# Optimization experiments

Hardware: AMD Instinct MI355X
Metric: run time of the kernel (lower is better)

## Reference

```python
import jax, jax.numpy as jnp
import numpy as np

N_NEAR = 16
BN_EPS = 1e-5


def fps(xyz, n_center):
    # farthest point sampling, deterministic start at index 0. xyz: [B,N,C]
    B, N, _ = xyz.shape
    dist0 = jnp.full((B, N), jnp.inf, dtype=xyz.dtype)
    far0 = jnp.zeros((B,), dtype=jnp.int32)

    def step(carry, _):
        dist, far = carry
        centroid = jnp.take_along_axis(xyz, far[:, None, None], axis=1)  # [B,1,C]
        d = jnp.sum((xyz - centroid) ** 2, axis=-1)                       # [B,N]
        dist = jnp.minimum(dist, d)
        nxt = jnp.argmax(dist, axis=-1).astype(jnp.int32)
        return (dist, nxt), far

    _, idxs = jax.lax.scan(step, (dist0, far0), None, length=n_center)
    return jnp.transpose(idxs)  # [B, n_center]


def knn(xyz, k):
    # k nearest neighbors (self included), xyz: [B,N,C] -> idx [B,N,k]
    sq = jnp.sum(xyz * xyz, axis=-1)
    d = sq[:, :, None] - 2.0 * jnp.einsum('bnc,bmc->bnm', xyz, xyz) + sq[:, None, :]
    _, idx = jax.lax.top_k(-d, k)
    return idx


def gather_points(x, idx):
    # x: [B,N,...], idx: [B,*dims] int -> [B,*dims,...]
    return jax.vmap(lambda xb, ib: xb[ib])(x, idx)


def conv_bn_relu(x, W, b, g, be):
    # x: [B,C,K,S]; 1x1 Conv2d + BatchNorm2d (training/batch stats) + ReLU
    y = jnp.einsum('oc,bcks->boks', W, x) + b[None, :, None, None]
    mean = jnp.mean(y, axis=(0, 2, 3), keepdims=True)
    var = jnp.mean((y - mean) ** 2, axis=(0, 2, 3), keepdims=True)  # biased var, as torch BN
    y = (y - mean) * jax.lax.rsqrt(var + BN_EPS)
    y = y * g[None, :, None, None] + be[None, :, None, None]
    return jax.nn.relu(y)


def setup_inputs() -> dict:
    key = jax.random.key(0)
    ks = jax.random.split(key, 8)
    B, N, EMB = 16, 2048, 64
    mlp = [64, 128, 256]
    in_ch = 2 + EMB
    inp = {
        'xy': jax.random.normal(ks[0], (B, 2, N), dtype=jnp.float32),
        'fea': jax.random.normal(ks[1], (B, EMB, N), dtype=jnp.float32),
    }
    last = in_ch
    for i, out in enumerate(mlp):
        inp[f'W{i+1}'] = 0.1 * jax.random.normal(ks[2 + i], (out, last), dtype=jnp.float32)
        inp[f'b{i+1}'] = jnp.zeros((out,), dtype=jnp.float32)
        inp[f'g{i+1}'] = jnp.ones((out,), dtype=jnp.float32)
        inp[f'be{i+1}'] = jnp.zeros((out,), dtype=jnp.float32)
        last = out
    return inp


def reference(xy, fea, W1, b1, g1, be1, W2, b2, g2, be2, W3, b3, g3, be3):
    B, _, N = xy.shape
    n_center = N // 2 + 1
    xyz = jnp.transpose(xy, (0, 2, 1))   # [B,N,2]
    f = jnp.transpose(fea, (0, 2, 1))    # [B,N,emb]

    fps_idx = fps(xyz, n_center)                      # [B,S]
    new_xyz = gather_points(xyz, fps_idx)             # [B,S,2]
    knn_idx = knn(xyz, N_NEAR)                        # [B,N,k]
    knn_of_fps = gather_points(knn_idx, fps_idx)      # [B,S,k]
    grouped_xyz = gather_points(xyz, knn_of_fps)      # [B,S,k,2]
    grouped_norm = grouped_xyz - new_xyz[:, :, None, :]
    grouped_f = gather_points(f, knn_of_fps)          # [B,S,k,emb]
    new_fea = jnp.concatenate([grouped_norm, grouped_f], axis=-1)  # [B,S,k,C]

    x = jnp.transpose(new_fea, (0, 3, 2, 1))          # [B,C,k,S]
    for (W, b, g, be) in ((W1, b1, g1, be1), (W2, b2, g2, be2), (W3, b3, g3, be3)):
        x = conv_bn_relu(x, W, b, g, be)
    out = jnp.max(x, axis=2)                          # [B,C_out,S]
    return jnp.transpose(new_xyz, (0, 2, 1)), out
```

## Files before the change

kernel.cpp:

```cpp
#include <hip/hip_runtime.h>
#include <math.h>

#define B_   16
#define N_   2048
#define S_   1025
#define K_   16
#define EMB_ 64
#define NF_  (B_ * S_ * K_)
#define NCH_ (NF_ / 64)

typedef float v2f __attribute__((ext_vector_type(2)));
typedef short bf16x8 __attribute__((ext_vector_type(8)));
typedef float f32x4 __attribute__((ext_vector_type(4)));

__device__ __forceinline__ unsigned short f2bf(float f) {
  unsigned u = __float_as_uint(f);
  u += 0x7fffu + ((u >> 16) & 1u);
  return (unsigned short)(u >> 16);
}

__global__ __launch_bounds__(256) __attribute__((amdgpu_waves_per_eu(1, 1)))
void fps_pk_kernel(const float* __restrict__ xy, const float* __restrict__ fea,
                   const float* __restrict__ W1,
                   const float* __restrict__ W2, const float* __restrict__ W3,
                   int* __restrict__ fps_idx, float* __restrict__ new_xyz,
                   float* __restrict__ out0, float* __restrict__ P,
                   unsigned short* __restrict__ W2b, unsigned short* __restrict__ W3b) {
  __shared__ float smem[8192];
  if (blockIdx.x < 16) {
    const int b = blockIdx.x;
    float2* lxy = reinterpret_cast<float2*>(smem);
    const int lane = threadIdx.x;
    const float* xb = xy + (size_t)b * 2 * N_;
    v2f pxp[16], pyp[16];
    float dist[32];
    if (lane < 64) {
      const float2* xb2 = (const float2*)xb;
      const float2* yb2 = (const float2*)(xb + N_);
#pragma unroll
      for (int q = 0; q < 16; ++q) {
        float2 x01 = xb2[lane * 16 + q];
        float2 y01 = yb2[lane * 16 + q];
        int p = lane * 32 + 2 * q;
        lxy[p] = make_float2(x01.x, y01.x);
        lxy[p + 1] = make_float2(x01.y, y01.y);
        pxp[q][0] = x01.x; pxp[q][1] = x01.y;
        pyp[q][0] = y01.x; pyp[q][1] = y01.y;
        dist[2 * q] = __builtin_inff();
        dist[2 * q + 1] = __builtin_inff();
      }
#pragma unroll
      for (int q = 0; q < 16; ++q) {
        asm volatile("" : "+v"(pxp[q]), "+v"(pyp[q]));
      }
    }
    __syncthreads();
    if (lane < 64) {
      int cur = 0;
      for (int t = 0; t < S_; ++t) {
        float2 c = lxy[cur];
        if (lane == 0) {
          fps_idx[b * S_ + t] = cur;
          new_xyz[(b * S_ + t) * 2 + 0] = c.x;
          new_xyz[(b * S_ + t) * 2 + 1] = c.y;
          out0[b * 2 * S_ + t] = c.x;
          out0[b * 2 * S_ + S_ + t] = c.y;
        }
        const float ncx = -c.x, ncy = -c.y;
        v2f ncx2; ncx2[0] = ncx; ncx2[1] = ncx;
        v2f ncy2; ncy2[0] = ncy; ncy2[1] = ncy;
#pragma unroll
        for (int q = 0; q < 16; ++q) {
          v2f dx, dy, sx, sy, dd;
          asm("v_pk_add_f32 %0, %1, %2" : "=v"(dx) : "v"(pxp[q]), "v"(ncx2));
          asm("v_pk_add_f32 %0, %1, %2" : "=v"(dy) : "v"(pyp[q]), "v"(ncy2));
          asm("v_pk_mul_f32 %0, %1, %1" : "=v"(sx) : "v"(dx));
          asm("v_pk_mul_f32 %0, %1, %1" : "=v"(sy) : "v"(dy));
          asm("v_pk_add_f32 %0, %1, %2" : "=v"(dd) : "v"(sx), "v"(sy));
          dist[2 * q] = fminf(dist[2 * q], dd[0]);
          dist[2 * q + 1] = fminf(dist[2 * q + 1], dd[1]);
        }
        float m1[16], m2[8], m3[4], m4[2];
#pragma unroll
        for (int j = 0; j < 16; ++j) m1[j] = fmaxf(dist[2 * j], dist[2 * j + 1]);
#pragma unroll
        for (int j = 0; j < 8; ++j) m2[j] = fmaxf(m1[2 * j], m1[2 * j + 1]);
#pragma unroll
        for (int j = 0; j < 4; ++j) m3[j] = fmaxf(m2[2 * j], m2[2 * j + 1]);
        m4[0] = fmaxf(m3[0], m3[1]);
        m4[1] = fmaxf(m3[2], m3[3]);
        const float lmax = fmaxf(m4[0], m4[1]);
        int xr = __float_as_int(lmax);
#define DPP_MAX_STEP(CTRL)                                                        \
        {                                                                         \
          int tmp_ = __builtin_amdgcn_update_dpp(xr, xr, (CTRL), 0xF, 0xF, false);\
          xr = __float_as_int(fmaxf(__int_as_float(xr), __int_as_float(tmp_)));   \
        }
        DPP_MAX_STEP(0x111)
        DPP_MAX_STEP(0x112)
        DPP_MAX_STEP(0x114)
        DPP_MAX_STEP(0x118)
        DPP_MAX_STEP(0x142)
        DPP_MAX_STEP(0x143)
#undef DPP_MAX_STEP
        const float g = __int_as_float(__builtin_amdgcn_readlane(xr, 63));
        int n = (m4[0] == g) ? 0 : 1;
        float c3 = (n & 1) ? m3[2] : m3[0];
        n = 2 * n + ((c3 == g) ? 0 : 1);
        float lo2 = (n & 1) ? m2[2] : m2[0];
        float hi2 = (n & 1) ? m2[6] : m2[4];
        float c2 = (n & 2) ? hi2 : lo2;
        n = 2 * n + ((c2 == g) ? 0 : 1);
        float a0 = (n & 1) ? m1[2] : m1[0];
        float a1 = (n & 1) ? m1[6] : m1[4];
        float a2 = (n & 1) ? m1[10] : m1[8];
        float a3 = (n & 1) ? m1[14] : m1[12];
        float b0 = (n & 2) ? a1 : a0;
        float b1 = (n & 2) ? a3 : a2;
        float c1 = (n & 4) ? b1 : b0;
        n = 2 * n + ((c1 == g) ? 0 : 1);
        float e0 = (n & 1) ? dist[2] : dist[0];
        float e1 = (n & 1) ? dist[6] : dist[4];
        float e2 = (n & 1) ? dist[10] : dist[8];
        float e3 = (n & 1) ? dist[14] : dist[12];
        float e4 = (n & 1) ? dist[18] : dist[16];
        float e5 = (n & 1) ? dist[22] : dist[20];
        float e6 = (n & 1) ? dist[26] : dist[24];
        float e7 = (n & 1) ? dist[30] : dist[28];
        float f0 = (n & 2) ? e1 : e0;
        float f1 = (n & 2) ? e3 : e2;
        float f2 = (n & 2) ? e5 : e4;
        float f3 = (n & 2) ? e7 : e6;
        float g0 = (n & 4) ? f1 : f0;
        float g1 = (n & 4) ? f3 : f2;
        float c0 = (n & 8) ? g1 : g0;
        const int lf = 2 * n + ((c0 == g) ? 0 : 1);
        unsigned long long mask = __ballot(lmax == g);
        int first = __ffsll(mask) - 1;
        cur = __builtin_amdgcn_readlane(lane * 32 + lf, first);
      }
    }
  } else if (blockIdx.x < 528) {
    const int bid = blockIdx.x - 16;
    const int t = threadIdx.x;
    const int b = bid >> 5;
    const int pt0 = (bid & 31) << 6;
    float* W1L = smem;
    float* feaL = smem + 4096;
#pragma unroll
    for (int p = 0; p < 16; ++p) {
      int idx = t + 256 * p;
      int c = idx >> 6, e = idx & 63;
      W1L[e * 64 + c] = W1[c * 66 + 2 + e];
      int r = (t >> 6) + 4 * p, cc = t & 63;
      feaL[r * 64 + cc] = fea[((size_t)b * 64 + r) * N_ + pt0 + cc];
    }
    __syncthreads();
    const int tpt = t & 15, tcq = t >> 4;
    float acc[4][4];
#pragma unroll
    for (int i = 0; i < 4; ++i)
#pragma unroll
      for (int j = 0; j < 4; ++j) acc[i][j] = 0.f;
    for (int e = 0; e < 64; ++e) {
      float4 a4 = *reinterpret_cast<const float4*>(&W1L[e * 64 + tcq * 4]);
      float4 b4 = *reinterpret_cast<const float4*>(&feaL[e * 64 + tpt * 4]);
      const float av[4] = {a4.x, a4.y, a4.z, a4.w};
      const float bvv[4] = {b4.x, b4.y, b4.z, b4.w};
#pragma unroll
      for (int i = 0; i < 4; ++i)
#pragma unroll
        for (int j = 0; j < 4; ++j) acc[i][j] = fmaf(av[i], bvv[j], acc[i][j]);
    }
#pragma unroll
    for (int j = 0; j < 4; ++j) {
      int pt = tpt * 4 + j;
      float4 v = {acc[0][j], acc[1][j], acc[2][j], acc[3][j]};
      *reinterpret_cast<float4*>(&P[((size_t)(b * N_ + pt0 + pt)) * 64 + tcq * 4]) = v;
    }
  } else {
    const int t = threadIdx.x;
    for (int i = t; i < 128 * 64; i += 256) W2b[i] = f2bf(W2[i]);
    for (int i = t; i < 256 * 128; i += 256) W3b[i] = f2bf(W3[i]);
  }
}

__global__ __launch_bounds__(256) void knn_kernel(const float* __restrict__ xy,
                                                  const int* __restrict__ fps_idx,
                                                  int* __restrict__ knn_sel) {
  const int b = blockIdx.y;
  __shared__ float2 lxy[N_];
  __shared__ double lsq[N_];
  const float* xb = xy + (size_t)b * 2 * N_;
  for (int p = threadIdx.x; p < N_; p += 256) {
    float x = xb[p], y = xb[N_ + p];
    lxy[p] = make_float2(x, y);
    lsq[p] = (double)x * (double)x + (double)y * (double)y;
  }
  __syncthreads();
  const int t = threadIdx.x;
  const int s = blockIdx.x * 8 + (t >> 5);
  if (s >= S_) return;
  const int oct = t & 31;
  const int p0 = fps_idx[b * S_ + s];
  float2 q = lxy[p0];
  const double xn = (double)q.x, yn = (double)q.y;
  const double sqn = lsq[p0];
  double d16[16];
  int i16[16];
#pragma unroll
  for (int j = 0; j < 16; ++j) { d16[j] = __builtin_inf(); i16[j] = 0x7fffffff; }
  const int mlo = oct * 64;
  for (int m0 = mlo; m0 < mlo + 64; m0 += 4) {
    double dd[4];
#pragma unroll
    for (int u = 0; u < 4; ++u) {
      float2 p = lxy[m0 + u];
      double dot = (double)p.x * xn + (double)p.y * yn;
      dd[u] = (sqn - 2.0 * dot) + lsq[m0 + u];
    }
#pragma unroll
    for (int u = 0; u < 4; ++u) {
      if (dd[u] < d16[15]) {
        double d = dd[u];
        int mi = m0 + u;
#pragma unroll
        for (int j = 15; j >= 1; --j) {
          bool shift = d < d16[j - 1];
          bool ins = d < d16[j];
          d16[j] = shift ? d16[j - 1] : (ins ? d : d16[j]);
          i16[j] = shift ? i16[j - 1] : (ins ? mi : i16[j]);
        }
        if (d < d16[0]) { d16[0] = d; i16[0] = mi; }
      }
    }
  }
#pragma unroll
  for (int w = 1; w <= 16; w <<= 1) {
    double nd[16]; int ni[16];
#pragma unroll
    for (int i = 0; i < 16; ++i) {
      double rd = __shfl_xor(d16[15 - i], w, 64);
      int ri = __shfl_xor(i16[15 - i], w, 64);
      bool takeR = (rd < d16[i]) || (rd == d16[i] && ri < i16[i]);
      nd[i] = takeR ? rd : d16[i];
      ni[i] = takeR ? ri : i16[i];
    }
#pragma unroll
    for (int i = 0; i < 16; ++i) { d16[i] = nd[i]; i16[i] = ni[i]; }
    if (w < 16) {
#pragma unroll
      for (int dstg = 8; dstg >= 1; dstg >>= 1) {
#pragma unroll
        for (int i = 0; i < 16; ++i) {
          if ((i & dstg) == 0) {
            int a = i, c = i + dstg;
            bool sw = (d16[a] > d16[c]) || (d16[a] == d16[c] && i16[a] > i16[c]);
            double tlo = sw ? d16[c] : d16[a];
            double thi = sw ? d16[a] : d16[c];
            int ulo = sw ? i16[c] : i16[a];
            int uhi = sw ? i16[a] : i16[c];
            d16[a] = tlo; d16[c] = thi; i16[a] = ulo; i16[c] = uhi;
          }
        }
      }
    }
  }
  if (oct == 0) {
    int* dst = knn_sel + ((size_t)b * S_ + s) * K_;
#pragma unroll
    for (int j = 0; j < 16; ++j) dst[j] = i16[j];
  }
}

__global__ __launch_bounds__(256) void yk1_kernel(const float* __restrict__ xy,
                                                  const int* __restrict__ knn_sel,
                                                  const float* __restrict__ new_xyz,
                                                  const float* __restrict__ P,
                                                  const float* __restrict__ W1,
                                                  const float* __restrict__ b1,
                                                  float* __restrict__ Y1) {
  __shared__ float w0s[64], w1s[64], bbs[64];
  const int t = threadIdx.x;
  if (t < 64) { w0s[t] = W1[t * 66 + 0]; w1s[t] = W1[t * 66 + 1]; bbs[t] = b1[t]; }
  __syncthreads();
  const int n = blockIdx.x * 256 + t;
  const int bs = n >> 4;
  const int b = bs / S_;
  const int nbr = knn_sel[n];
  const float dx = xy[(size_t)b * 2 * N_ + nbr] - new_xyz[bs * 2 + 0];
  const float dy = xy[(size_t)b * 2 * N_ + N_ + nbr] - new_xyz[bs * 2 + 1];
  const float* prow = &P[((size_t)(b * N_ + nbr)) * 64];
  for (int c4 = 0; c4 < 64; c4 += 4) {
    float4 p4 = *reinterpret_cast<const float4*>(&prow[c4]);
    float v0 = p4.x + w0s[c4 + 0] * dx + w1s[c4 + 0] * dy + bbs[c4 + 0];
    float v1 = p4.y + w0s[c4 + 1] * dx + w1s[c4 + 1] * dy + bbs[c4 + 1];
    float v2 = p4.z + w0s[c4 + 2] * dx + w1s[c4 + 2] * dy + bbs[c4 + 2];
    float v3 = p4.w + w0s[c4 + 3] * dx + w1s[c4 + 3] * dy + bbs[c4 + 3];
    Y1[(size_t)(c4 + 0) * NF_ + n] = v0;
    Y1[(size_t)(c4 + 1) * NF_ + n] = v1;
    Y1[(size_t)(c4 + 2) * NF_ + n] = v2;
    Y1[(size_t)(c4 + 3) * NF_ + n] = v3;
  }
}

__global__ __launch_bounds__(256) void rowstats_kernel(const float* __restrict__ Y,
                                                       float* __restrict__ parts) {
  const int r = blockIdx.x & 63;
  const int qtr = blockIdx.x >> 6;
  const int QLEN = NF_ / 4;
  const float* seg = Y + (size_t)r * NF_ + (size_t)qtr * QLEN;
  double s = 0.0, s2 = 0.0;
  for (int i = threadIdx.x * 4; i < QLEN; i += 1024) {
    float4 v = *reinterpret_cast<const float4*>(&seg[i]);
    double dx = v.x, dy = v.y, dz = v.z, dw = v.w;
    s += (dx + dy) + (dz + dw);
    s2 = fma(dx, dx, s2); s2 = fma(dy, dy, s2);
    s2 = fma(dz, dz, s2); s2 = fma(dw, dw, s2);
  }
  __shared__ double sh[256], sh2[256];
  sh[threadIdx.x] = s; sh2[threadIdx.x] = s2;
  __syncthreads();
  for (int o = 128; o > 0; o >>= 1) {
    if (threadIdx.x < o) {
      sh[threadIdx.x] += sh[threadIdx.x + o];
      sh2[threadIdx.x] += sh2[threadIdx.x + o];
    }
    __syncthreads();
  }
  if (threadIdx.x == 0) {
    parts[(size_t)qtr * 128 + r] = (float)sh[0];
    parts[(size_t)qtr * 128 + 64 + r] = (float)sh2[0];
  }
}

__global__ void redabsch_kernel(const float* __restrict__ parts, int P, int M,
                                const float* __restrict__ g, const float* __restrict__ be,
                                float* __restrict__ A, float* __restrict__ D) {
  int m = threadIdx.x;
  if (m >= M) return;
  double a = 0.0, b = 0.0;
  for (int p = 0; p < P; ++p) {
    a += (double)parts[(size_t)p * 2 * M + m];
    b += (double)parts[(size_t)p * 2 * M + M + m];
  }
  double mu = a * (1.0 / NF_);
  double var = b * (1.0 / NF_) - mu * mu;
  double aa = (double)g[m] / sqrt(var + 1e-5);
  A[m] = (float)aa;
  D[m] = (float)((double)be[m] - aa * mu);
}

__device__ __forceinline__ float rowsum16(float v) {
#define RADD(CTRL) { int tm_ = __builtin_amdgcn_update_dpp(0, __float_as_int(v), (CTRL), 0xF, 0xF, true); \
                     v += __int_as_float(tm_); }
  RADD(0x111) RADD(0x112) RADD(0x114) RADD(0x118)
#undef RADD
  return v;
}

__global__ __launch_bounds__(256) void passA_mfma_kernel(
    const float* __restrict__ Y1, const unsigned short* __restrict__ W2b,
    const float* __restrict__ A1v, const float* __restrict__ Bc1v,
    float* __restrict__ parts) {
  __shared__ float ab1[128];
  __shared__ __align__(16) unsigned short x1b[64 * 64];
  const int t = threadIdx.x;
  const int w = t >> 6, L = t & 63;
  if (t < 128) ab1[t] = (t < 64) ? A1v[t] : Bc1v[t - 64];
  bf16x8 w2f[2][2];
#pragma unroll
  for (int rb = 0; rb < 2; ++rb)
#pragma unroll
    for (int ks = 0; ks < 2; ++ks) {
      int row = (2 * w + rb) * 16 + (L & 15);
      int koff = ks * 32 + (L >> 4) * 8;
      w2f[rb][ks] = *reinterpret_cast<const bf16x8*>(&W2b[row * 64 + koff]);
    }
  float vs[2][4], vq[2][4];
#pragma unroll
  for (int rb = 0; rb < 2; ++rb)
#pragma unroll
    for (int r = 0; r < 4; ++r) { vs[rb][r] = 0.f; vq[rb][r] = 0.f; }
  char* x1c = reinterpret_cast<char*>(x1b);
  for (int ch = blockIdx.x; ch < NCH_; ch += 512) {
    const size_t n0 = (size_t)ch * 64;
    __syncthreads();
#pragma unroll
    for (int e = 0; e < 8; ++e) {
      int k0 = 2 * (w + 4 * e);
      float y0 = Y1[(size_t)k0 * NF_ + n0 + L];
      float y1 = Y1[(size_t)(k0 + 1) * NF_ + n0 + L];
      float v0 = fmaxf(fmaf(y0, ab1[k0], ab1[64 + k0]), 0.f);
      float v1 = fmaxf(fmaf(y1, ab1[k0 + 1], ab1[64 + k0 + 1]), 0.f);
      unsigned pk = (unsigned)f2bf(v0) | ((unsigned)f2bf(v1) << 16);
      *reinterpret_cast<unsigned*>(&x1c[L * 128 + ((2 * k0) ^ ((L & 7) << 4))]) = pk;
    }
    __syncthreads();
#pragma unroll
    for (int rb = 0; rb < 2; ++rb) {
      f32x4 acc2[4];
#pragma unroll
      for (int cb = 0; cb < 4; ++cb) acc2[cb][0] = acc2[cb][1] = acc2[cb][2] = acc2[cb][3] = 0.f;
#pragma unroll
      for (int ks = 0; ks < 2; ++ks)
#pragma unroll
        for (int cb = 0; cb < 4; ++cb) {
          int n = cb * 16 + (L & 15);
          int koff = ks * 32 + (L >> 4) * 8;
          bf16x8 bfr = *reinterpret_cast<const bf16x8*>(&x1c[n * 128 + ((2 * koff) ^ ((n & 7) << 4))]);
          acc2[cb] = __builtin_amdgcn_mfma_f32_16x16x32_bf16(w2f[rb][ks], bfr, acc2[cb], 0, 0, 0);
        }
#pragma unroll
      for (int cb = 0; cb < 4; ++cb)
#pragma unroll
        for (int r = 0; r < 4; ++r) {
          float y = acc2[cb][r];
          vs[rb][r] += y;
          vq[rb][r] = fmaf(y, y, vq[rb][r]);
        }
    }
  }
#pragma unroll
  for (int rb = 0; rb < 2; ++rb)
#pragma unroll
    for (int r = 0; r < 4; ++r) {
      float s = rowsum16(vs[rb][r]);
      float q = rowsum16(vq[rb][r]);
      if ((L & 15) == 15) {
        int row = (2 * w + rb) * 16 + (L >> 4) * 4 + r;
        parts[(size_t)blockIdx.x * 256 + row] = s;
        parts[(size_t)blockIdx.x * 256 + 128 + row] = q;
      }
    }
}

__global__ __launch_bounds__(256) void passB_mfma_kernel(
    const float* __restrict__ Y1,
    const unsigned short* __restrict__ W2b, const unsigned short* __restrict__ W3b,
    const float* __restrict__ A1v, const float* __restrict__ Bc1v,
    const float* __restrict__ A2v, const float* __restrict__ D2v,
    float* __restrict__ parts) {
  __shared__ float ab1[128];
  __shared__ __align__(16) unsigned short x1b[64 * 64];
  __shared__ __align__(16) unsigned short x2b[64 * 128];
  const int t = threadIdx.x;
  const int w = t >> 6, L = t & 63;
  if (t < 128) ab1[t] = (t < 64) ? A1v[t] : Bc1v[t - 64];
  bf16x8 w3f[4][4];
#pragma unroll
  for (int rb = 0; rb < 4; ++rb)
#pragma unroll
    for (int ks = 0; ks < 4; ++ks) {
      int row = (4 * w + rb) * 16 + (L & 15);
      int koff = ks * 32 + (L >> 4) * 8;
      w3f[rb][ks] = *reinterpret_cast<const bf16x8*>(&W3b[row * 128 + koff]);
    }
  bf16x8 w2f[2][2];
#pragma unroll
  for (int rb = 0; rb < 2; ++rb)
#pragma unroll
    for (int ks = 0; ks < 2; ++ks) {
      int row = (2 * w + rb) * 16 + (L & 15);
      int koff = ks * 32 + (L >> 4) * 8;
      w2f[rb][ks] = *reinterpret_cast<const bf16x8*>(&W2b[row * 64 + koff]);
    }
  float vs[4][4], vq[4][4];
#pragma unroll
  for (int rb = 0; rb < 4; ++rb)
#pragma unroll
    for (int r = 0; r < 4; ++r) { vs[rb][r] = 0.f; vq[rb][r] = 0.f; }
  char* x1c = reinterpret_cast<char*>(x1b);
  char* x2c = reinterpret_cast<char*>(x2b);
  for (int ch = blockIdx.x; ch < NCH_; ch += 256) {
    const size_t n0 = (size_t)ch * 64;
    __syncthreads();
#pragma unroll
    for (int e = 0; e < 8; ++e) {
      int k0 = 2 * (w + 4 * e);
      float y0 = Y1[(size_t)k0 * NF_ + n0 + L];
      float y1 = Y1[(size_t)(k0 + 1) * NF_ + n0 + L];
      float v0 = fmaxf(fmaf(y0, ab1[k0], ab1[64 + k0]), 0.f);
      float v1 = fmaxf(fmaf(y1, ab1[k0 + 1], ab1[64 + k0 + 1]), 0.f);
      unsigned pk = (unsigned)f2bf(v0) | ((unsigned)f2bf(v1) << 16);
      *reinterpret_cast<unsigned*>(&x1c[L * 128 + ((2 * k0) ^ ((L & 7) << 4))]) = pk;
    }
    __syncthreads();
#pragma unroll
    for (int rb = 0; rb < 2; ++rb) {
      f32x4 acc2[4];
#pragma unroll
      for (int cb = 0; cb < 4; ++cb) acc2[cb][0] = acc2[cb][1] = acc2[cb][2] = acc2[cb][3] = 0.f;
#pragma unroll
      for (int ks = 0; ks < 2; ++ks)
#pragma unroll
        for (int cb = 0; cb < 4; ++cb) {
          int n = cb * 16 + (L & 15);
          int koff = ks * 32 + (L >> 4) * 8;
          bf16x8 bfr = *reinterpret_cast<const bf16x8*>(&x1c[n * 128 + ((2 * koff) ^ ((n & 7) << 4))]);
          acc2[cb] = __builtin_amdgcn_mfma_f32_16x16x32_bf16(w2f[rb][ks], bfr, acc2[cb], 0, 0, 0);
        }
#pragma unroll
      for (int cb = 0; cb < 4; ++cb) {
        int n = cb * 16 + (L & 15);
        int kbase = (2 * w + rb) * 16 + (L >> 4) * 4;
#pragma unroll
        for (int rp = 0; rp < 2; ++rp) {
          int r0 = 2 * rp;
          float a0 = A2v[kbase + r0], d0 = D2v[kbase + r0];
          float a1 = A2v[kbase + r0 + 1], d1 = D2v[kbase + r0 + 1];
          float v0 = fmaxf(fmaf(acc2[cb][r0], a0, d0), 0.f);
          float v1 = fmaxf(fmaf(acc2[cb][r0 + 1], a1, d1), 0.f);
          unsigned pk = (unsigned)f2bf(v0) | ((unsigned)f2bf(v1) << 16);
          int k0 = kbase + r0;
          *reinterpret_cast<unsigned*>(&x2c[n * 256 + ((2 * k0) ^ ((n & 7) << 4))]) = pk;
        }
      }
    }
    __syncthreads();
    bf16x8 b3[4][4];
#pragma unroll
    for (int cb = 0; cb < 4; ++cb)
#pragma unroll
      for (int ks = 0; ks < 4; ++ks) {
        int n = cb * 16 + (L & 15);
        int koff = ks * 32 + (L >> 4) * 8;
        b3[cb][ks] = *reinterpret_cast<const bf16x8*>(&x2c[n * 256 + ((2 * koff) ^ ((n & 7) << 4))]);
      }
#pragma unroll
    for (int rb = 0; rb < 4; ++rb) {
      f32x4 acc3[4];
#pragma unroll
      for (int cb = 0; cb < 4; ++cb) acc3[cb][0] = acc3[cb][1] = acc3[cb][2] = acc3[cb][3] = 0.f;
#pragma unroll
      for (int ks = 0; ks < 4; ++ks)
#pragma unroll
        for (int cb = 0; cb < 4; ++cb)
          acc3[cb] = __builtin_amdgcn_mfma_f32_16x16x32_bf16(w3f[rb][ks], b3[cb][ks], acc3[cb], 0, 0, 0);
#pragma unroll
      for (int cb = 0; cb < 4; ++cb)
#pragma unroll
        for (int r = 0; r < 4; ++r) {
          float y = acc3[cb][r];
          vs[rb][r] += y;
          vq[rb][r] = fmaf(y, y, vq[rb][r]);
        }
    }
  }
#pragma unroll
  for (int rb = 0; rb < 4; ++rb)
#pragma unroll
    for (int r = 0; r < 4; ++r) {
      float s = rowsum16(vs[rb][r]);
      float q = rowsum16(vq[rb][r]);
      if ((L & 15) == 15) {
        int row = (4 * w + rb) * 16 + (L >> 4) * 4 + r;
        parts[(size_t)blockIdx.x * 512 + row] = s;
        parts[(size_t)blockIdx.x * 512 + 256 + row] = q;
      }
    }
}

__global__ __launch_bounds__(256) void final_mfma_kernel(
    const float* __restrict__ Y1,
    const unsigned short* __restrict__ W2b,
    const unsigned short* __restrict__ W3b,
    const float* __restrict__ A1v, const float* __restrict__ Bc1v,
    const float* __restrict__ A2v, const float* __restrict__ D2v,
    const float* __restrict__ A3v, const float* __restrict__ D3v,
    float* __restrict__ out1) {
  __shared__ float ab1[128];
  __shared__ __align__(16) unsigned short x1b[64 * 64];
  __shared__ __align__(16) unsigned short x2b[64 * 128];
  const int t = threadIdx.x;
  const int w = t >> 6, L = t & 63;
  if (t < 128) ab1[t] = (t < 64) ? A1v[t] : Bc1v[t - 64];
  bf16x8 w3f[4][4];
#pragma unroll
  for (int rb = 0; rb < 4; ++rb)
#pragma unroll
    for (int ks = 0; ks < 4; ++ks) {
      int row = (4 * w + rb) * 16 + (L & 15);
      int koff = ks * 32 + (L >> 4) * 8;
      w3f[rb][ks] = *reinterpret_cast<const bf16x8*>(&W3b[row * 128 + koff]);
    }
  bf16x8 w2f[2][2];
#pragma unroll
  for (int rb = 0; rb < 2; ++rb)
#pragma unroll
    for (int ks = 0; ks < 2; ++ks) {
      int row = (2 * w + rb) * 16 + (L & 15);
      int koff = ks * 32 + (L >> 4) * 8;
      w2f[rb][ks] = *reinterpret_cast<const bf16x8*>(&W2b[row * 64 + koff]);
    }
  char* x1c = reinterpret_cast<char*>(x1b);
  char* x2c = reinterpret_cast<char*>(x2b);
  for (int ch = blockIdx.x; ch < NCH_; ch += 512) {
    const size_t n0 = (size_t)ch * 64;
    __syncthreads();
#pragma unroll
    for (int e = 0; e < 8; ++e) {
      int k0 = 2 * (w + 4 * e);
      float y0 = Y1[(size_t)k0 * NF_ + n0 + L];
      float y1 = Y1[(size_t)(k0 + 1) * NF_ + n0 + L];
      float v0 = fmaxf(fmaf(y0, ab1[k0], ab1[64 + k0]), 0.f);
      float v1 = fmaxf(fmaf(y1, ab1[k0 + 1], ab1[64 + k0 + 1]), 0.f);
      unsigned pk = (unsigned)f2bf(v0) | ((unsigned)f2bf(v1) << 16);
      *reinterpret_cast<unsigned*>(&x1c[L * 128 + ((2 * k0) ^ ((L & 7) << 4))]) = pk;
    }
    __syncthreads();
#pragma unroll
    for (int rb = 0; rb < 2; ++rb) {
      f32x4 acc2[4];
#pragma unroll
      for (int cb = 0; cb < 4; ++cb) acc2[cb][0] = acc2[cb][1] = acc2[cb][2] = acc2[cb][3] = 0.f;
#pragma unroll
      for (int ks = 0; ks < 2; ++ks)
#pragma unroll
        for (int cb = 0; cb < 4; ++cb) {
          int n = cb * 16 + (L & 15);
          int koff = ks * 32 + (L >> 4) * 8;
          bf16x8 bfr = *reinterpret_cast<const bf16x8*>(&x1c[n * 128 + ((2 * koff) ^ ((n & 7) << 4))]);
          acc2[cb] = __builtin_amdgcn_mfma_f32_16x16x32_bf16(w2f[rb][ks], bfr, acc2[cb], 0, 0, 0);
        }
#pragma unroll
      for (int cb = 0; cb < 4; ++cb) {
        int n = cb * 16 + (L & 15);
        int kbase = (2 * w + rb) * 16 + (L >> 4) * 4;
#pragma unroll
        for (int rp = 0; rp < 2; ++rp) {
          int r0 = 2 * rp;
          float a0 = A2v[kbase + r0], d0 = D2v[kbase + r0];
          float a1 = A2v[kbase + r0 + 1], d1 = D2v[kbase + r0 + 1];
          float v0 = fmaxf(fmaf(acc2[cb][r0], a0, d0), 0.f);
          float v1 = fmaxf(fmaf(acc2[cb][r0 + 1], a1, d1), 0.f);
          unsigned pk = (unsigned)f2bf(v0) | ((unsigned)f2bf(v1) << 16);
          int k0 = kbase + r0;
          *reinterpret_cast<unsigned*>(&x2c[n * 256 + ((2 * k0) ^ ((n & 7) << 4))]) = pk;
        }
      }
    }
    __syncthreads();
    bf16x8 b3[4][4];
#pragma unroll
    for (int cb = 0; cb < 4; ++cb)
#pragma unroll
      for (int ks = 0; ks < 4; ++ks) {
        int n = cb * 16 + (L & 15);
        int koff = ks * 32 + (L >> 4) * 8;
        b3[cb][ks] = *reinterpret_cast<const bf16x8*>(&x2c[n * 256 + ((2 * koff) ^ ((n & 7) << 4))]);
      }
#pragma unroll
    for (int rb = 0; rb < 4; ++rb) {
      f32x4 acc3[4];
#pragma unroll
      for (int cb = 0; cb < 4; ++cb) acc3[cb][0] = acc3[cb][1] = acc3[cb][2] = acc3[cb][3] = 0.f;
#pragma unroll
      for (int ks = 0; ks < 4; ++ks)
#pragma unroll
        for (int cb = 0; cb < 4; ++cb)
          acc3[cb] = __builtin_amdgcn_mfma_f32_16x16x32_bf16(w3f[rb][ks], b3[cb][ks], acc3[cb], 0, 0, 0);
      int rowbase = (4 * w + rb) * 16 + (L >> 4) * 4;
#pragma unroll
      for (int cb = 0; cb < 4; ++cb) {
#pragma unroll
        for (int r = 0; r < 4; ++r) {
          float v = fmaf(acc3[cb][r], A3v[rowbase + r], D3v[rowbase + r]);
          int xi = __float_as_int(v);
#define RMAX(CTRL) { int tm_ = __builtin_amdgcn_update_dpp(xi, xi, (CTRL), 0xF, 0xF, false); \
                     xi = __float_as_int(fmaxf(__int_as_float(xi), __int_as_float(tm_))); }
          RMAX(0x111) RMAX(0x112) RMAX(0x114) RMAX(0x118)
#undef RMAX
          if ((L & 15) == 15) {
            int row = rowbase + r;
            int bs = ch * 4 + cb;
            int b = bs / S_;
            int s = bs - b * S_;
            out1[((size_t)(b * 256 + row)) * S_ + s] = fmaxf(__int_as_float(xi), 0.f);
          }
        }
      }
    }
  }
}

__global__ void diag_kernel(float* out, float v) {
  if (threadIdx.x == 0 && blockIdx.x == 0) out[0] = v;
}

extern "C" void kernel_launch(void* const* d_in, const int* in_sizes, int n_in,
                              void* d_out, int out_size, void* d_ws, size_t ws_size,
                              hipStream_t stream) {
  const float* xy  = (const float*)d_in[0];
  const float* fea = (const float*)d_in[1];
  const float* W1  = (const float*)d_in[2];
  const float* b1  = (const float*)d_in[3];
  const float* g1  = (const float*)d_in[4];
  const float* be1 = (const float*)d_in[5];
  const float* W2  = (const float*)d_in[6];
  const float* g2  = (const float*)d_in[8];
  const float* be2 = (const float*)d_in[9];
  const float* W3  = (const float*)d_in[10];
  const float* g3  = (const float*)d_in[12];
  const float* be3 = (const float*)d_in[13];
  float* out = (float*)d_out;
  float* out1 = out + B_ * 2 * S_;

  char* w = (char*)d_ws;
  size_t off = 0;
  auto take = [&](size_t bytes) -> void* {
    void* p = w + off;
    off += (bytes + 255) & ~(size_t)255;
    return p;
  };
  int*    fps_idx = (int*)take((size_t)B_ * S_ * 4);
  float*  new_xyz = (float*)take((size_t)B_ * S_ * 2 * 4);
  int*    knn_sel = (int*)take((size_t)NF_ * 4);
  float*  P       = (float*)take((size_t)B_ * N_ * 64 * 4);
  float*  Y1      = (float*)take((size_t)64 * NF_ * 4);
  float*  parts1  = (float*)take((size_t)4 * 128 * 4);
  float*  A1      = (float*)take(64 * 4);
  float*  Bc1     = (float*)take(64 * 4);
  float*  partsA  = (float*)take((size_t)512 * 256 * 4);
  float*  A2      = (float*)take(128 * 4);
  float*  D2      = (float*)take(128 * 4);
  float*  partsB  = (float*)take((size_t)256 * 512 * 4);
  float*  A3      = (float*)take(256 * 4);
  float*  D3      = (float*)take(256 * 4);
  unsigned short* W2b = (unsigned short*)take((size_t)128 * 64 * 2);
  unsigned short* W3b = (unsigned short*)take((size_t)256 * 128 * 2);

  if (off > ws_size) {
    diag_kernel<<<1, 64, 0, stream>>>(out, (float)(ws_size >> 20));
    return;
  }

  fps_pk_kernel<<<16 + 512 + 1, 256, 0, stream>>>(xy, fea, W1, W2, W3,
                                                  fps_idx, new_xyz, out, P, W2b, W3b);
  knn_kernel<<<dim3((S_ + 7) / 8, B_), 256, 0, stream>>>(xy, fps_idx, knn_sel);
  yk1_kernel<<<NF_ / 256, 256, 0, stream>>>(xy, knn_sel, new_xyz, P, W1, b1, Y1);

  rowstats_kernel<<<256, 256, 0, stream>>>(Y1, parts1);
  redabsch_kernel<<<1, 64, 0, stream>>>(parts1, 4, 64, g1, be1, A1, Bc1);

  passA_mfma_kernel<<<512, 256, 0, stream>>>(Y1, W2b, A1, Bc1, partsA);
  redabsch_kernel<<<1, 128, 0, stream>>>(partsA, 512, 128, g2, be2, A2, D2);

  passB_mfma_kernel<<<256, 256, 0, stream>>>(Y1, W2b, W3b, A1, Bc1, A2, D2, partsB);
  redabsch_kernel<<<1, 256, 0, stream>>>(partsB, 256, 256, g3, be3, A3, D3);

  final_mfma_kernel<<<512, 256, 0, stream>>>(Y1, W2b, W3b, A1, Bc1, A2, D2, A3, D3, out1);
}
```

Measured before the change: 1.343 ms.

## Store intermediates in bf16 and fold final max into passB via min/max

The P projection and the Y1 layer-1 activations are now stored as packed bf16 instead of fp32, halving the traffic for the yk1, rowstats, passA and passB kernels. passB also records per-group max and min of the raw layer-3 MFMA outputs. Those go into a small M3 buffer, so the final kernel only picks max or min by the sign of the BN scale and applies the affine and ReLU. This removes the third full recomputation of layers 2 and 3 in final_mfma_kernel. The cost is extra bf16 rounding of Y1, P and the stored max/min values, which could shift accuracy, plus extra DPP reductions in passB.

```diff
diff --git a/kernel.cpp b/kernel.cpp
--- a/kernel.cpp
+++ b/kernel.cpp
@@ -8,6 +8,7 @@
 #define EMB_ 64
 #define NF_  (B_ * S_ * K_)
 #define NCH_ (NF_ / 64)
+#define NBS_ (NCH_ * 4)
 
 typedef float v2f __attribute__((ext_vector_type(2)));
 typedef short bf16x8 __attribute__((ext_vector_type(8)));
@@ -18,13 +19,15 @@
   u += 0x7fffu + ((u >> 16) & 1u);
   return (unsigned short)(u >> 16);
 }
+__device__ __forceinline__ float bfl(unsigned pk) { return __uint_as_float((pk & 0xffffu) << 16); }
+__device__ __forceinline__ float bfh(unsigned pk) { return __uint_as_float(pk & 0xffff0000u); }
 
 __global__ __launch_bounds__(256) __attribute__((amdgpu_waves_per_eu(1, 1)))
 void fps_pk_kernel(const float* __restrict__ xy, const float* __restrict__ fea,
                    const float* __restrict__ W1,
                    const float* __restrict__ W2, const float* __restrict__ W3,
                    int* __restrict__ fps_idx, float* __restrict__ new_xyz,
-                   float* __restrict__ out0, float* __restrict__ P,
+                   float* __restrict__ out0, unsigned* __restrict__ Pp,
                    unsigned short* __restrict__ W2b, unsigned short* __restrict__ W3b) {
   __shared__ float smem[8192];
   if (blockIdx.x < 16) {
@@ -175,8 +178,11 @@
 #pragma unroll
     for (int j = 0; j < 4; ++j) {
       int pt = tpt * 4 + j;
-      float4 v = {acc[0][j], acc[1][j], acc[2][j], acc[3][j]};
-      *reinterpret_cast<float4*>(&P[((size_t)(b * N_ + pt0 + pt)) * 64 + tcq * 4]) = v;
+      unsigned lo = (unsigned)f2bf(acc[0][j]) | ((unsigned)f2bf(acc[1][j]) << 16);
+      unsigned hi = (unsigned)f2bf(acc[2][j]) | ((unsigned)f2bf(acc[3][j]) << 16);
+      unsigned* dst = &Pp[((size_t)(b * N_ + pt0 + pt)) * 32 + tcq * 2];
+      dst[0] = lo;
+      dst[1] = hi;
     }
   } else {
     const int t = threadIdx.x;
@@ -276,10 +282,10 @@
 __global__ __launch_bounds__(256) void yk1_kernel(const float* __restrict__ xy,
                                                   const int* __restrict__ knn_sel,
                                                   const float* __restrict__ new_xyz,
-                                                  const float* __restrict__ P,
+                                                  const unsigned* __restrict__ Pp,
                                                   const float* __restrict__ W1,
                                                   const float* __restrict__ b1,
-                                                  float* __restrict__ Y1) {
+                                                  unsigned* __restrict__ Y1p) {
   __shared__ float w0s[64], w1s[64], bbs[64];
   const int t = threadIdx.x;
   if (t < 64) { w0s[t] = W1[t * 66 + 0]; w1s[t] = W1[t * 66 + 1]; bbs[t] = b1[t]; }
@@ -290,48 +296,67 @@
   const int nbr = knn_sel[n];
   const float dx = xy[(size_t)b * 2 * N_ + nbr] - new_xyz[bs * 2 + 0];
   const float dy = xy[(size_t)b * 2 * N_ + N_ + nbr] - new_xyz[bs * 2 + 1];
-  const float* prow = &P[((size_t)(b * N_ + nbr)) * 64];
-  for (int c4 = 0; c4 < 64; c4 += 4) {
-    float4 p4 = *reinterpret_cast<const float4*>(&prow[c4]);
-    float v0 = p4.x + w0s[c4 + 0] * dx + w1s[c4 + 0] * dy + bbs[c4 + 0];
-    float v1 = p4.y + w0s[c4 + 1] * dx + w1s[c4 + 1] * dy + bbs[c4 + 1];
-    float v2 = p4.z + w0s[c4 + 2] * dx + w1s[c4 + 2] * dy + bbs[c4 + 2];
-    float v3 = p4.w + w0s[c4 + 3] * dx + w1s[c4 + 3] * dy + bbs[c4 + 3];
-    Y1[(size_t)(c4 + 0) * NF_ + n] = v0;
-    Y1[(size_t)(c4 + 1) * NF_ + n] = v1;
-    Y1[(size_t)(c4 + 2) * NF_ + n] = v2;
-    Y1[(size_t)(c4 + 3) * NF_ + n] = v3;
-  }
-}
-
-__global__ __launch_bounds__(256) void rowstats_kernel(const float* __restrict__ Y,
+  const unsigned* prow = &Pp[((size_t)(b * N_ + nbr)) * 32];
+#pragma unroll 8
+  for (int j = 0; j < 32; ++j) {
+    unsigned pj = prow[j];
+    int c = 2 * j;
+    float v0 = bfl(pj) + w0s[c] * dx + w1s[c] * dy + bbs[c];
+    float v1 = bfh(pj) + w0s[c + 1] * dx + w1s[c + 1] * dy + bbs[c + 1];
+    Y1p[(size_t)j * NF_ + n] = (unsigned)f2bf(v0) | ((unsigned)f2bf(v1) << 16);
+  }
+}
+
+__global__ __launch_bounds__(256) void rowstats_kernel(const unsigned* __restrict__ Y1p,
                                                        float* __restrict__ parts) {
-  const int r = blockIdx.x & 63;
-  const int qtr = blockIdx.x >> 6;
-  const int QLEN = NF_ / 4;
-  const float* seg = Y + (size_t)r * NF_ + (size_t)qtr * QLEN;
-  double s = 0.0, s2 = 0.0;
-  for (int i = threadIdx.x * 4; i < QLEN; i += 1024) {
-    float4 v = *reinterpret_cast<const float4*>(&seg[i]);
-    double dx = v.x, dy = v.y, dz = v.z, dw = v.w;
-    s += (dx + dy) + (dz + dw);
-    s2 = fma(dx, dx, s2); s2 = fma(dy, dy, s2);
-    s2 = fma(dz, dz, s2); s2 = fma(dw, dw, s2);
-  }
-  __shared__ double sh[256], sh2[256];
-  sh[threadIdx.x] = s; sh2[threadIdx.x] = s2;
+  const int j = blockIdx.x & 31;
+  const int seg = blockIdx.x >> 5;
+  const int SEG = NF_ / 8;
+  const unsigned* p = Y1p + (size_t)j * NF_ + (size_t)seg * SEG;
+  double s0 = 0, q0 = 0, s1 = 0, q1 = 0;
+  for (int i = threadIdx.x; i < SEG; i += 256) {
+    unsigned pk = p[i];
+    double a = (double)bfl(pk), b = (double)bfh(pk);
+    s0 += a; q0 = fma(a, a, q0);
+    s1 += b; q1 = fma(b, b, q1);
+  }
+  __shared__ double sh[4][256];
+  sh[0][threadIdx.x] = s0; sh[1][threadIdx.x] = q0;
+  sh[2][threadIdx.x] = s1; sh[3][threadIdx.x] = q1;
   __syncthreads();
   for (int o = 128; o > 0; o >>= 1) {
     if (threadIdx.x < o) {
-      sh[threadIdx.x] += sh[threadIdx.x + o];
-      sh2[threadIdx.x] += sh2[threadIdx.x + o];
+#pragma unroll
+      for (int u = 0; u < 4; ++u) sh[u][threadIdx.x] += sh[u][threadIdx.x + o];
     }
     __syncthreads();
   }
   if (threadIdx.x == 0) {
-    parts[(size_t)qtr * 128 + r] = (float)sh[0];
-    parts[(size_t)qtr * 128 + 64 + r] = (float)sh2[0];
-  }
+    float* dst = parts + (size_t)(j * 8 + seg) * 4;
+    dst[0] = (float)sh[0][0];
+    dst[1] = (float)sh[2][0];
+    dst[2] = (float)sh[1][0];
+    dst[3] = (float)sh[3][0];
+  }
+}
+
+__global__ void redabsch1_kernel(const float* __restrict__ parts,
+                                 const float* __restrict__ g, const float* __restrict__ be,
+                                 float* __restrict__ A, float* __restrict__ D) {
+  int m = threadIdx.x;
+  if (m >= 64) return;
+  int j = m >> 1, par = m & 1;
+  double a = 0.0, b = 0.0;
+  for (int seg = 0; seg < 8; ++seg) {
+    const float* src = parts + (size_t)(j * 8 + seg) * 4;
+    a += (double)src[par];
+    b += (double)src[2 + par];
+  }
+  double mu = a * (1.0 / NF_);
+  double var = b * (1.0 / NF_) - mu * mu;
+  double aa = (double)g[m] / sqrt(var + 1e-5);
+  A[m] = (float)aa;
+  D[m] = (float)((double)be[m] - aa * mu);
 }
 
 __global__ void redabsch_kernel(const float* __restrict__ parts, int P, int M,
@@ -359,8 +384,21 @@
   return v;
 }
 
+__device__ __forceinline__ void stage_x1(const unsigned* Y1p, const float* ab1, char* x1c,
+                                         size_t n0, int w, int L) {
+#pragma unroll
+  for (int e = 0; e < 8; ++e) {
+    int k0 = 2 * (w + 4 * e);
+    unsigned pkv = Y1p[(size_t)(k0 >> 1) * NF_ + n0 + L];
+    float v0 = fmaxf(fmaf(bfl(pkv), ab1[k0], ab1[64 + k0]), 0.f);
+    float v1 = fmaxf(fmaf(bfh(pkv), ab1[k0 + 1], ab1[64 + k0 + 1]), 0.f);
+    unsigned pk = (unsigned)f2bf(v0) | ((unsigned)f2bf(v1) << 16);
+    *reinterpret_cast<unsigned*>(&x1c[L * 128 + ((2 * k0) ^ ((L & 7) << 4))]) = pk;
+  }
+}
+
 __global__ __launch_bounds__(256) void passA_mfma_kernel(
-    const float* __restrict__ Y1, const unsigned short* __restrict__ W2b,
+    const unsigned* __restrict__ Y1p, const unsigned short* __restrict__ W2b,
     const float* __restrict__ A1v, const float* __restrict__ Bc1v,
     float* __restrict__ parts) {
   __shared__ float ab1[128];
@@ -386,16 +424,7 @@
   for (int ch = blockIdx.x; ch < NCH_; ch += 512) {
     const size_t n0 = (size_t)ch * 64;
     __syncthreads();
-#pragma unroll
-    for (int e = 0; e < 8; ++e) {
-      int k0 = 2 * (w + 4 * e);
-      float y0 = Y1[(size_t)k0 * NF_ + n0 + L];
-      float y1 = Y1[(size_t)(k0 + 1) * NF_ + n0 + L];
-      float v0 = fmaxf(fmaf(y0, ab1[k0], ab1[64 + k0]), 0.f);
-      float v1 = fmaxf(fmaf(y1, ab1[k0 + 1], ab1[64 + k0 + 1]), 0.f);
-      unsigned pk = (unsigned)f2bf(v0) | ((unsigned)f2bf(v1) << 16);
-      *reinterpret_cast<unsigned*>(&x1c[L * 128 + ((2 * k0) ^ ((L & 7) << 4))]) = pk;
-    }
+    stage_x1(Y1p, ab1, x1c, n0, w, L);
     __syncthreads();
 #pragma unroll
     for (int rb = 0; rb < 2; ++rb) {
@@ -436,11 +465,11 @@
 }
 
 __global__ __launch_bounds__(256) void passB_mfma_kernel(
-    const float* __restrict__ Y1,
+    const unsigned* __restrict__ Y1p,
     const unsigned short* __restrict__ W2b, const unsigned short* __restrict__ W3b,
     const float* __restrict__ A1v, const float* __restrict__ Bc1v,
     const float* __restrict__ A2v, const float* __restrict__ D2v,
-    float* __restrict__ parts) {
+    float* __restrict__ parts, unsigned* __restrict__ M3) {
   __shared__ float ab1[128];
   __shared__ __align__(16) unsigned short x1b[64 * 64];
   __shared__ __align__(16) unsigned short x2b[64 * 128];
@@ -475,16 +504,7 @@
   for (int ch = blockIdx.x; ch < NCH_; ch += 256) {
     const size_t n0 = (size_t)ch * 64;
     __syncthreads();
-#pragma unroll
-    for (int e = 0; e < 8; ++e) {
-      int k0 = 2 * (w + 4 * e);
-      float y0 = Y1[(size_t)k0 * NF_ + n0 + L];
-      float y1 = Y1[(size_t)(k0 + 1) * NF_ + n0 + L];
-      float v0 = fmaxf(fmaf(y0, ab1[k0], ab1[64 + k0]), 0.f);
-      float v1 = fmaxf(fmaf(y1, ab1[k0 + 1], ab1[64 + k0 + 1]), 0.f);
-      unsigned pk = (unsigned)f2bf(v0) | ((unsigned)f2bf(v1) << 16);
-      *reinterpret_cast<unsigned*>(&x1c[L * 128 + ((2 * k0) ^ ((L & 7) << 4))]) = pk;
-    }
+    stage_x1(Y1p, ab1, x1c, n0, w, L);
     __syncthreads();
 #pragma unroll
     for (int rb = 0; rb < 2; ++rb) {
@@ -545,6 +565,31 @@
           vs[rb][r] += y;
           vq[rb][r] = fmaf(y, y, vq[rb][r]);
         }
+      {
+        int rowbase = (4 * w + rb) * 16 + (L >> 4) * 4;
+#pragma unroll
+        for (int cb = 0; cb < 4; ++cb) {
+#pragma unroll
+          for (int r = 0; r < 4; ++r) {
+            float v = acc3[cb][r];
+            int xi = __float_as_int(v), xm = __float_as_int(v);
+#define RMAX(CTRL) { int tm_ = __builtin_amdgcn_update_dpp(xi, xi, (CTRL), 0xF, 0xF, false); \
+                     xi = __float_as_int(fmaxf(__int_as_float(xi), __int_as_float(tm_))); }
+#define RMIN(CTRL) { int tm_ = __builtin_amdgcn_update_dpp(xm, xm, (CTRL), 0xF, 0xF, false); \
+                     xm = __float_as_int(fminf(__int_as_float(xm), __int_as_float(tm_))); }
+            RMAX(0x111) RMAX(0x112) RMAX(0x114) RMAX(0x118)
+            RMIN(0x111) RMIN(0x112) RMIN(0x114) RMIN(0x118)
+#undef RMAX
+#undef RMIN
+            if ((L & 15) == 15) {
+              int row = rowbase + r;
+              int bs = ch * 4 + cb;
+              M3[(size_t)row * NBS_ + bs] =
+                  (unsigned)f2bf(__int_as_float(xi)) | ((unsigned)f2bf(__int_as_float(xm)) << 16);
+            }
+          }
+        }
+      }
     }
   }
 #pragma unroll
@@ -561,127 +606,18 @@
     }
 }
 
-__global__ __launch_bounds__(256) void final_mfma_kernel(
-    const float* __restrict__ Y1,
-    const unsigned short* __restrict__ W2b,
-    const unsigned short* __restrict__ W3b,
-    const float* __restrict__ A1v, const float* __restrict__ Bc1v,
-    const float* __restrict__ A2v, const float* __restrict__ D2v,
-    const float* __restrict__ A3v, const float* __restrict__ D3v,
-    float* __restrict__ out1) {
-  __shared__ float ab1[128];
-  __shared__ __align__(16) unsigned short x1b[64 * 64];
-  __shared__ __align__(16) unsigned short x2b[64 * 128];
-  const int t = threadIdx.x;
-  const int w = t >> 6, L = t & 63;
-  if (t < 128) ab1[t] = (t < 64) ? A1v[t] : Bc1v[t - 64];
-  bf16x8 w3f[4][4];
-#pragma unroll
-  for (int rb = 0; rb < 4; ++rb)
-#pragma unroll
-    for (int ks = 0; ks < 4; ++ks) {
-      int row = (4 * w + rb) * 16 + (L & 15);
-      int koff = ks * 32 + (L >> 4) * 8;
-      w3f[rb][ks] = *reinterpret_cast<const bf16x8*>(&W3b[row * 128 + koff]);
-    }
-  bf16x8 w2f[2][2];
-#pragma unroll
-  for (int rb = 0; rb < 2; ++rb)
-#pragma unroll
-    for (int ks = 0; ks < 2; ++ks) {
-      int row = (2 * w + rb) * 16 + (L & 15);
-      int koff = ks * 32 + (L >> 4) * 8;
-      w2f[rb][ks] = *reinterpret_cast<const bf16x8*>(&W2b[row * 64 + koff]);
-    }
-  char* x1c = reinterpret_cast<char*>(x1b);
-  char* x2c = reinterpret_cast<char*>(x2b);
-  for (int ch = blockIdx.x; ch < NCH_; ch += 512) {
-    const size_t n0 = (size_t)ch * 64;
-    __syncthreads();
-#pragma unroll
-    for (int e = 0; e < 8; ++e) {
-      int k0 = 2 * (w + 4 * e);
-      float y0 = Y1[(size_t)k0 * NF_ + n0 + L];
-      float y1 = Y1[(size_t)(k0 + 1) * NF_ + n0 + L];
-      float v0 = fmaxf(fmaf(y0, ab1[k0], ab1[64 + k0]), 0.f);
-      float v1 = fmaxf(fmaf(y1, ab1[k0 + 1], ab1[64 + k0 + 1]), 0.f);
-      unsigned pk = (unsigned)f2bf(v0) | ((unsigned)f2bf(v1) << 16);
-      *reinterpret_cast<unsigned*>(&x1c[L * 128 + ((2 * k0) ^ ((L & 7) << 4))]) = pk;
-    }
-    __syncthreads();
-#pragma unroll
-    for (int rb = 0; rb < 2; ++rb) {
-      f32x4 acc2[4];
-#pragma unroll
-      for (int cb = 0; cb < 4; ++cb) acc2[cb][0] = acc2[cb][1] = acc2[cb][2] = acc2[cb][3] = 0.f;
-#pragma unroll
-      for (int ks = 0; ks < 2; ++ks)
-#pragma unroll
-        for (int cb = 0; cb < 4; ++cb) {
-          int n = cb * 16 + (L & 15);
-          int koff = ks * 32 + (L >> 4) * 8;
-          bf16x8 bfr = *reinterpret_cast<const bf16x8*>(&x1c[n * 128 + ((2 * koff) ^ ((n & 7) << 4))]);
-          acc2[cb] = __builtin_amdgcn_mfma_f32_16x16x32_bf16(w2f[rb][ks], bfr, acc2[cb], 0, 0, 0);
-        }
-#pragma unroll
-      for (int cb = 0; cb < 4; ++cb) {
-        int n = cb * 16 + (L & 15);
-        int kbase = (2 * w + rb) * 16 + (L >> 4) * 4;
-#pragma unroll
-        for (int rp = 0; rp < 2; ++rp) {
-          int r0 = 2 * rp;
-          float a0 = A2v[kbase + r0], d0 = D2v[kbase + r0];
-          float a1 = A2v[kbase + r0 + 1], d1 = D2v[kbase + r0 + 1];
-          float v0 = fmaxf(fmaf(acc2[cb][r0], a0, d0), 0.f);
-          float v1 = fmaxf(fmaf(acc2[cb][r0 + 1], a1, d1), 0.f);
-          unsigned pk = (unsigned)f2bf(v0) | ((unsigned)f2bf(v1) << 16);
-          int k0 = kbase + r0;
-          *reinterpret_cast<unsigned*>(&x2c[n * 256 + ((2 * k0) ^ ((n & 7) << 4))]) = pk;
-        }
-      }
-    }
-    __syncthreads();
-    bf16x8 b3[4][4];
-#pragma unroll
-    for (int cb = 0; cb < 4; ++cb)
-#pragma unroll
-      for (int ks = 0; ks < 4; ++ks) {
-        int n = cb * 16 + (L & 15);
-        int koff = ks * 32 + (L >> 4) * 8;
-        b3[cb][ks] = *reinterpret_cast<const bf16x8*>(&x2c[n * 256 + ((2 * koff) ^ ((n & 7) << 4))]);
-      }
-#pragma unroll
-    for (int rb = 0; rb < 4; ++rb) {
-      f32x4 acc3[4];
-#pragma unroll
-      for (int cb = 0; cb < 4; ++cb) acc3[cb][0] = acc3[cb][1] = acc3[cb][2] = acc3[cb][3] = 0.f;
-#pragma unroll
-      for (int ks = 0; ks < 4; ++ks)
-#pragma unroll
-        for (int cb = 0; cb < 4; ++cb)
-          acc3[cb] = __builtin_amdgcn_mfma_f32_16x16x32_bf16(w3f[rb][ks], b3[cb][ks], acc3[cb], 0, 0, 0);
-      int rowbase = (4 * w + rb) * 16 + (L >> 4) * 4;
-#pragma unroll
-      for (int cb = 0; cb < 4; ++cb) {
-#pragma unroll
-        for (int r = 0; r < 4; ++r) {
-          float v = fmaf(acc3[cb][r], A3v[rowbase + r], D3v[rowbase + r]);
-          int xi = __float_as_int(v);
-#define RMAX(CTRL) { int tm_ = __builtin_amdgcn_update_dpp(xi, xi, (CTRL), 0xF, 0xF, false); \
-                     xi = __float_as_int(fmaxf(__int_as_float(xi), __int_as_float(tm_))); }
-          RMAX(0x111) RMAX(0x112) RMAX(0x114) RMAX(0x118)
-#undef RMAX
-          if ((L & 15) == 15) {
-            int row = rowbase + r;
-            int bs = ch * 4 + cb;
-            int b = bs / S_;
-            int s = bs - b * S_;
-            out1[((size_t)(b * 256 + row)) * S_ + s] = fmaxf(__int_as_float(xi), 0.f);
-          }
-        }
-      }
-    }
-  }
+__global__ __launch_bounds__(256) void final_small_kernel(
+    const unsigned* __restrict__ M3, const float* __restrict__ A3,
+    const float* __restrict__ D3, float* __restrict__ out1) {
+  int gid = blockIdx.x * 256 + threadIdx.x;
+  int row = gid / NBS_, bs = gid - row * NBS_;
+  unsigned pk = M3[gid];
+  float vmax = bfl(pk);
+  float vmin = bfh(pk);
+  float a = A3[row];
+  float v = (a >= 0.f) ? vmax : vmin;
+  int b = bs / S_, s = bs - b * S_;
+  out1[((size_t)(b * 256 + row)) * S_ + s] = fmaxf(fmaf(v, a, D3[row]), 0.f);
 }
 
 __global__ void diag_kernel(float* out, float v) {
@@ -713,22 +649,23 @@
     off += (bytes + 255) & ~(size_t)255;
     return p;
   };
-  int*    fps_idx = (int*)take((size_t)B_ * S_ * 4);
-  float*  new_xyz = (float*)take((size_t)B_ * S_ * 2 * 4);
-  int*    knn_sel = (int*)take((size_t)NF_ * 4);
-  float*  P       = (float*)take((size_t)B_ * N_ * 64 * 4);
-  float*  Y1      = (float*)take((size_t)64 * NF_ * 4);
-  float*  parts1  = (float*)take((size_t)4 * 128 * 4);
-  float*  A1      = (float*)take(64 * 4);
-  float*  Bc1     = (float*)take(64 * 4);
-  float*  partsA  = (float*)take((size_t)512 * 256 * 4);
-  float*  A2      = (float*)take(128 * 4);
-  float*  D2      = (float*)take(128 * 4);
-  float*  partsB  = (float*)take((size_t)256 * 512 * 4);
-  float*  A3      = (float*)take(256 * 4);
-  float*  D3      = (float*)take(256 * 4);
+  int*      fps_idx = (int*)take((size_t)B_ * S_ * 4);
+  float*    new_xyz = (float*)take((size_t)B_ * S_ * 2 * 4);
+  int*      knn_sel = (int*)take((size_t)NF_ * 4);
+  unsigned* Pp      = (unsigned*)take((size_t)B_ * N_ * 32 * 4);
+  unsigned* Y1p     = (unsigned*)take((size_t)32 * NF_ * 4);
+  float*    parts1  = (float*)take((size_t)256 * 4 * 4);
+  float*    A1      = (float*)take(64 * 4);
+  float*    Bc1     = (float*)take(64 * 4);
+  float*    partsA  = (float*)take((size_t)512 * 256 * 4);
+  float*    A2      = (float*)take(128 * 4);
+  float*    D2      = (float*)take(128 * 4);
+  float*    partsB  = (float*)take((size_t)256 * 512 * 4);
+  float*    A3      = (float*)take(256 * 4);
+  float*    D3      = (float*)take(256 * 4);
   unsigned short* W2b = (unsigned short*)take((size_t)128 * 64 * 2);
   unsigned short* W3b = (unsigned short*)take((size_t)256 * 128 * 2);
+  unsigned* M3      = (unsigned*)take((size_t)256 * NBS_ * 4);
 
   if (off > ws_size) {
     diag_kernel<<<1, 64, 0, stream>>>(out, (float)(ws_size >> 20));
@@ -736,18 +673,18 @@
   }
 
   fps_pk_kernel<<<16 + 512 + 1, 256, 0, stream>>>(xy, fea, W1, W2, W3,
-                                                  fps_idx, new_xyz, out, P, W2b, W3b);
+                                                  fps_idx, new_xyz, out, Pp, W2b, W3b);
   knn_kernel<<<dim3((S_ + 7) / 8, B_), 256, 0, stream>>>(xy, fps_idx, knn_sel);
-  yk1_kernel<<<NF_ / 256, 256, 0, stream>>>(xy, knn_sel, new_xyz, P, W1, b1, Y1);
-
-  rowstats_kernel<<<256, 256, 0, stream>>>(Y1, parts1);
-  redabsch_kernel<<<1, 64, 0, stream>>>(parts1, 4, 64, g1, be1, A1, Bc1);
-
-  passA_mfma_kernel<<<512, 256, 0, stream>>>(Y1, W2b, A1, Bc1, partsA);
+  yk1_kernel<<<NF_ / 256, 256, 0, stream>>>(xy, knn_sel, new_xyz, Pp, W1, b1, Y1p);
+
+  rowstats_kernel<<<256, 256, 0, stream>>>(Y1p, parts1);
+  redabsch1_kernel<<<1, 64, 0, stream>>>(parts1, g1, be1, A1, Bc1);
+
+  passA_mfma_kernel<<<512, 256, 0, stream>>>(Y1p, W2b, A1, Bc1, partsA);
   redabsch_kernel<<<1, 128, 0, stream>>>(partsA, 512, 128, g2, be2, A2, D2);
 
-  passB_mfma_kernel<<<256, 256, 0, stream>>>(Y1, W2b, W3b, A1, Bc1, A2, D2, partsB);
+  passB_mfma_kernel<<<256, 256, 0, stream>>>(Y1p, W2b, W3b, A1, Bc1, A2, D2, partsB, M3);
   redabsch_kernel<<<1, 256, 0, stream>>>(partsB, 256, 256, g3, be3, A3, D3);
 
-  final_mfma_kernel<<<512, 256, 0, stream>>>(Y1, W2b, W3b, A1, Bc1, A2, D2, A3, D3, out1);
-}
+  final_small_kernel<<<(256 * NBS_) / 256, 256, 0, stream>>>(M3, A3, D3, out1);
+}
```

Result: no change. 1.351 ms (+0.6%).
